# Optimization experiments

Hardware: AMD Instinct MI355X
Metric: run time of the kernel (lower is better)

Reference implementation:

```python
import jax, jax.numpy as jnp
import numpy as np

D = 2  # NUM_DIM (spatial dimension)


def _mlp(x, params, activate_final=False):
    n = len(params)
    for i, (w, b) in enumerate(params):
        x = x @ w + b
        if i < n - 1 or activate_final:
            x = jnp.tanh(x)
    return x


def _glorot(key, shape):
    fan_in, fan_out = shape[0], shape[-1]
    lim = np.sqrt(6.0 / (fan_in + fan_out)).astype(np.float32)
    return jax.random.uniform(key, shape, jnp.float32, -lim, lim)


def setup_inputs() -> dict:
    key = jax.random.key(0)
    ks = iter(jax.random.split(key, 40))
    B, N, M, K, P, C = 4, 32, 64, 16, 128, 2
    AW, TW, W = 64, 256, 128
    inp = {}
    inp['phase_coords'] = jax.random.normal(next(ks), (B, N, 2 * D), jnp.float32)
    inp['boundary_coords'] = jax.random.normal(next(ks), (B, M, 2 * D), jnp.float32)
    inp['boundary'] = jax.random.uniform(next(ks), (B, M), jnp.float32)
    inp['boundary_weights'] = jax.random.uniform(next(ks), (B, M), jnp.float32)
    inp['position_coords'] = jax.random.normal(next(ks), (B, P, D), jnp.float32)
    inp['sigma'] = jax.random.uniform(next(ks), (B, P, C), jnp.float32)
    inp['velocity_coords'] = jax.random.normal(next(ks), (B, K, D), jnp.float32)
    inp['velocity_weights'] = jax.random.uniform(next(ks), (B, K), jnp.float32)
    inp['scattering_kernel'] = jax.random.uniform(next(ks), (B, N, K), jnp.float32)
    inp['self_scattering_kernel'] = jax.random.uniform(next(ks), (B, K, K), jnp.float32)
    # attention MLP: input 2*D + 2 (coords ++ local frame) -> [64, 64, 1]
    inp['aw0'] = _glorot(next(ks), (2 * D + 2, AW)); inp['ab0'] = jnp.zeros((AW,), jnp.float32)
    inp['aw1'] = _glorot(next(ks), (AW, AW)); inp['ab1'] = jnp.zeros((AW,), jnp.float32)
    inp['aw2'] = _glorot(next(ks), (AW, 1)); inp['ab2'] = jnp.zeros((1,), jnp.float32)
    # transport MLP: input 4*D + C -> [256, 256, 128], activate_final=True
    inp['tw0'] = _glorot(next(ks), (4 * D + C, TW)); inp['tb0'] = jnp.zeros((TW,), jnp.float32)
    inp['tw1'] = _glorot(next(ks), (TW, TW)); inp['tb1'] = jnp.zeros((TW,), jnp.float32)
    inp['tw2'] = _glorot(next(ks), (TW, W)); inp['tb2'] = jnp.zeros((W,), jnp.float32)
    # scattering modules: res_block_depth=2 -> one stacked layer + one final layer
    inp['sw0'] = _glorot(next(ks), (W, W))
    inp['sb0'] = jax.random.uniform(next(ks), (W,), jnp.float32, -0.1, 0.1)
    inp['sw1'] = _glorot(next(ks), (W, W))
    inp['sb1'] = jax.random.uniform(next(ks), (W,), jnp.float32, -0.1, 0.1)
    inp['out_w'] = jax.random.uniform(next(ks), (W,), jnp.float32, -0.1, 0.1)
    return inp


def _forward(phase_coords, boundary_coords, boundary, boundary_weights,
             position_coords, sigma, velocity_coords, velocity_weights,
             scattering_kernel, self_scattering_kernel,
             aw0, ab0, aw1, ab1, aw2, ab2,
             tw0, tb0, tw1, tb1, tw2, tb2,
             sw0, sb0, sw1, sb1, out_w):
    B, N, _ = phase_coords.shape
    M = boundary_coords.shape[1]
    K = velocity_coords.shape[1]
    P = position_coords.shape[1]
    C = sigma.shape[-1]
    K1 = K + 1  # phase velocity v plus the Nv quadrature velocities

    x, v = phase_coords[..., :D], phase_coords[..., D:]          # (B,N,D)
    xp, vp = boundary_coords[..., :D], boundary_coords[..., D:]  # (B,M,D)

    # all velocities at which the transport MLP is evaluated: (B,N,K1,D)
    vall = jnp.concatenate(
        [v[:, :, None, :],
         jnp.broadcast_to(velocity_coords[:, None, :, :], (B, N, K, D))], axis=2)

    # ---- CoefficientNet (geometry-masked MLP attention over coeff positions) ----
    coords = jnp.concatenate(
        [jnp.broadcast_to(x[:, :, None, :], (B, N, K1, D)), vall], axis=-1)  # (B,N,K1,2D)
    ang_g = vall / jnp.sqrt(jnp.sum(vall ** 2, axis=-1, keepdims=True) + 1e-16)
    rel = x[:, :, None, :] - position_coords[:, None, :, :]                 # (B,N,P,D)
    rel_dist = jnp.sqrt(jnp.sum(rel ** 2, axis=-1) + 1e-16)                 # (B,N,P)
    pos_local = jnp.einsum('bnpd,bnkd->bnkp', rel, ang_g)                   # (B,N,K1,P)
    ang_local = pos_local / (rel_dist[:, :, None, :] + 1e-8)
    frames = jnp.stack([ang_local, pos_local], axis=-1)                     # (B,N,K1,P,2)
    qk = jnp.concatenate(
        [jnp.broadcast_to(coords[:, :, :, None, :], (B, N, K1, P, 2 * D)), frames], axis=-1)
    logits = _mlp(qk, [(aw0, ab0), (aw1, ab1), (aw2, ab2)])[..., 0]         # (B,N,K1,P)
    attn_w = jax.nn.softmax(jnp.where(pos_local > 0, logits, -1e30), axis=-1)
    coeff = jnp.exp(-jnp.einsum('bnkp,bpc->bnkc', attn_w, sigma))           # (B,N,K1,C)

    # ---- TransportModule: MLP + exp over (B,N,M,K1) ----
    t_in = jnp.concatenate([
        jnp.broadcast_to(x[:, :, None, None, :], (B, N, M, K1, D)),
        jnp.broadcast_to(vall[:, :, None, :, :], (B, N, M, K1, D)),
        jnp.broadcast_to(xp[:, None, :, None, :], (B, N, M, K1, D)),
        jnp.broadcast_to(vp[:, None, :, None, :], (B, N, M, K1, D)),
        jnp.broadcast_to(coeff[:, :, None, :, :], (B, N, M, K1, C)),
    ], axis=-1)
    g = jnp.exp(_mlp(t_in, [(tw0, tb0), (tw1, tb1), (tw2, tb2)], activate_final=True))
    act_v = g[:, :, :, 0, :]       # (B,N,M,W)  at the phase velocity
    act_vstar = g[:, :, :, 1:, :]  # (B,N,M,K,W) at the quadrature velocities

    rw_v = (1.0 - scattering_kernel) * velocity_weights[:, None, :]        # (B,N,K)
    rw_vs = (1.0 - self_scattering_kernel) * velocity_weights[:, None, :]  # (B,K,K)

    def scat_v(act, sw, sb):
        res = jnp.einsum('bnk,bnmkw->bnmw', rw_v, act)
        return jnp.tanh(jnp.einsum('iw,bnmw->bnmi', sw, res) + sb)

    def scat_vs(act, sw, sb):
        res = jnp.einsum('bij,bnmjw->bnmiw', rw_vs, act)
        return jnp.tanh(jnp.einsum('iw,bnmkw->bnmki', sw, res) + sb)

    # layer_stack block (res_block_depth - 1 = 1 layer, shared params within the layer)
    new_v = act_v + scat_v(act_vstar, sw0, sb0)
    act_vstar = act_vstar + scat_vs(act_vstar, sw0, sb0)
    act_v = new_v
    # final scattering module (fresh params) updating act_v with res_weights_v
    green = act_v + scat_v(act_vstar, sw1, sb1)

    gdot = jnp.einsum('bnmw,w->bnm', green, out_w)
    # quadrature over boundary points
    return jnp.einsum('bnm,bm->bn', gdot, boundary * boundary_weights)


def reference(phase_coords, boundary_coords, boundary, boundary_weights,
              position_coords, sigma, velocity_coords, velocity_weights,
              scattering_kernel, self_scattering_kernel,
              aw0, ab0, aw1, ab1, aw2, ab2,
              tw0, tb0, tw1, tb1, tw2, tb2,
              sw0, sb0, sw1, sb1, out_w):
    return _forward(phase_coords, boundary_coords, boundary, boundary_weights,
                    position_coords, sigma, velocity_coords, velocity_weights,
                    scattering_kernel, self_scattering_kernel,
                    aw0, ab0, aw1, ab1, aw2, ab2,
                    tw0, tb0, tw1, tb1, tw2, tb2,
                    sw0, sb0, sw1, sb1, out_w)
```

## Files before the change

### kernel.cpp

```cpp
#include <hip/hip_runtime.h>
#include <hip/hip_bf16.h>

#define BB 4
#define NN 32
#define MM 64
#define KK 16
#define KK1 17
#define PP 128
#define CC 2

typedef unsigned short ushort_t;
typedef unsigned int uint32;
typedef __attribute__((ext_vector_type(8))) short bhalf8;
typedef __attribute__((ext_vector_type(4))) float floatx4;

__device__ __forceinline__ float fast_tanh(float x) {
    float e = __expf(2.0f * x);
    return 1.0f - 2.0f / (e + 1.0f);
}
__device__ __forceinline__ ushort_t f2b(float f) {
    uint32 u = __float_as_uint(f);
    return (ushort_t)((u + 0x8000u) >> 16);
}
__device__ __forceinline__ float b2f(ushort_t h) {
    return __uint_as_float(((uint32)h) << 16);
}

__global__ void prep_kernel(const float* __restrict__ tw0, const float* __restrict__ tw1,
                            const float* __restrict__ tw2, const float* __restrict__ sw0,
                            const float* __restrict__ sw1, const float* __restrict__ aw0,
                            const float* __restrict__ aw1, const float* __restrict__ tb0,
                            const float* __restrict__ bcoord,
                            ushort_t* __restrict__ W1t, ushort_t* __restrict__ W2t,
                            ushort_t* __restrict__ S0t, ushort_t* __restrict__ S1t,
                            ushort_t* __restrict__ W0a, ushort_t* __restrict__ W1a,
                            ushort_t* __restrict__ w_ws) {
    int i = blockIdx.x * 256 + threadIdx.x;
    if (i < 65536) {
        int nn = i >> 8, k = i & 255;
        W1t[i] = f2b(tw1[k * 256 + nn]);
    } else if (i < 98304) {
        int j = i - 65536; int nn = j >> 8, k = j & 255;
        W2t[j] = f2b(tw2[k * 128 + nn]);
    } else if (i < 114688) {
        S0t[i - 98304] = f2b(sw0[i - 98304]);
    } else if (i < 131072) {
        S1t[i - 114688] = f2b(sw1[i - 114688]);
    } else if (i < 133120) {
        int j = i - 131072; int nn = j >> 5, k = j & 31;
        W0a[j] = (k < 6) ? f2b(aw0[k * 64 + nn]) : (ushort_t)0;
    } else if (i < 137216) {
        int j = i - 133120; int nn = j >> 6, k = j & 63;
        W1a[j] = f2b(aw1[k * 64 + nn]);
    } else if (i < 202752) {
        int j = i - 137216;
        int m = j >> 8, c = j & 255;
        float v = bcoord[m * 4 + 0] * tw0[4 * 256 + c]
                + bcoord[m * 4 + 1] * tw0[5 * 256 + c]
                + bcoord[m * 4 + 2] * tw0[6 * 256 + c]
                + bcoord[m * 4 + 3] * tw0[7 * 256 + c]
                + tb0[c];
        w_ws[j] = f2b(v);
    }
}

#define AH0S 72

__global__ __launch_bounds__(128, 4) void attn_kernel(
    const float* __restrict__ phase, const float* __restrict__ posc,
    const float* __restrict__ sigma, const float* __restrict__ velc,
    const ushort_t* __restrict__ W0a, const ushort_t* __restrict__ W1a,
    const float* __restrict__ ab0, const float* __restrict__ ab1,
    const float* __restrict__ aw2, const float* __restrict__ ab2,
    const float* __restrict__ tw0, ushort_t* __restrict__ u_ws)
{
    __shared__ __align__(16) ushort_t sAH[128 * AH0S];
    __shared__ float sPL[128];
    __shared__ float sLG[128];
    __shared__ float s_red[8];

    const int tid = threadIdx.x;
    const int wave = tid >> 6;
    const int lane = tid & 63;
    const int lrow = lane & 15;
    const int lkg  = lane >> 4;

    const int blk = blockIdx.x;
    const int b = blk / (NN * KK1);
    const int rem = blk % (NN * KK1);
    const int n = rem / KK1;
    const int k = rem % KK1;

    float x0, x1, va0, va1;
    {
        const int p = tid;
        x0 = phase[(b * NN + n) * 4 + 0];
        x1 = phase[(b * NN + n) * 4 + 1];
        if (k == 0) { va0 = phase[(b * NN + n) * 4 + 2]; va1 = phase[(b * NN + n) * 4 + 3]; }
        else { va0 = velc[(b * KK + (k - 1)) * 2 + 0]; va1 = velc[(b * KK + (k - 1)) * 2 + 1]; }
        const float inv = rsqrtf(va0 * va0 + va1 * va1 + 1e-16f);
        const float ag0 = va0 * inv, ag1 = va1 * inv;
        const float px = posc[(b * PP + p) * 2 + 0];
        const float py = posc[(b * PP + p) * 2 + 1];
        const float r0 = x0 - px, r1 = x1 - py;
        const float rd = sqrtf(r0 * r0 + r1 * r1 + 1e-16f);
        const float pl = r0 * ag0 + r1 * ag1;
        const float al = pl / (rd + 1e-8f);
        sPL[p] = pl;
        bhalf8 f0;
        f0[0] = (short)f2b(x0); f0[1] = (short)f2b(x1);
        f0[2] = (short)f2b(va0); f0[3] = (short)f2b(va1);
        f0[4] = (short)f2b(al); f0[5] = (short)f2b(pl);
        f0[6] = 0; f0[7] = 0;
        bhalf8 z = {0, 0, 0, 0, 0, 0, 0, 0};
        *(bhalf8*)&sAH[p * 32 + 0] = f0;
        *(bhalf8*)&sAH[p * 32 + 8] = z;
        *(bhalf8*)&sAH[p * 32 + 16] = z;
        *(bhalf8*)&sAH[p * 32 + 24] = z;
    }
    __syncthreads();

    {
        float b0v[4];
        #pragma unroll
        for (int j = 0; j < 4; ++j) b0v[j] = ab0[j * 16 + lrow];
        bhalf8 a[4];
        #pragma unroll
        for (int mtl = 0; mtl < 4; ++mtl)
            a[mtl] = *(const bhalf8*)&sAH[(wave * 64 + mtl * 16 + lrow) * 32 + lkg * 8];
        __syncthreads();
        #pragma unroll
        for (int j = 0; j < 4; ++j) {
            bhalf8 bf = *(const bhalf8*)(W0a + (j * 16 + lrow) * 32 + lkg * 8);
            #pragma unroll
            for (int mtl = 0; mtl < 4; ++mtl) {
                floatx4 c = {0.f, 0.f, 0.f, 0.f};
                c = __builtin_amdgcn_mfma_f32_16x16x32_bf16(a[mtl], bf, c, 0, 0, 0);
                #pragma unroll
                for (int q = 0; q < 4; ++q) {
                    int row = wave * 64 + mtl * 16 + lkg * 4 + q;
                    sAH[row * AH0S + j * 16 + lrow] = f2b(fast_tanh(c[q] + b0v[j]));
                }
            }
        }
    }
    __syncthreads();

    {
        float b1v[4], w2v[4];
        #pragma unroll
        for (int j = 0; j < 4; ++j) { b1v[j] = ab1[j * 16 + lrow]; w2v[j] = aw2[j * 16 + lrow]; }
        bhalf8 a0[4], a1[4];
        #pragma unroll
        for (int mtl = 0; mtl < 4; ++mtl) {
            int base = (wave * 64 + mtl * 16 + lrow) * AH0S;
            a0[mtl] = *(const bhalf8*)&sAH[base + lkg * 8];
            a1[mtl] = *(const bhalf8*)&sAH[base + 32 + lkg * 8];
        }
        float s[4][4];
        #pragma unroll
        for (int mtl = 0; mtl < 4; ++mtl)
            #pragma unroll
            for (int q = 0; q < 4; ++q) s[mtl][q] = 0.0f;
        #pragma unroll
        for (int j = 0; j < 4; ++j) {
            bhalf8 bf0 = *(const bhalf8*)(W1a + (j * 16 + lrow) * 64 + lkg * 8);
            bhalf8 bf1 = *(const bhalf8*)(W1a + (j * 16 + lrow) * 64 + 32 + lkg * 8);
            #pragma unroll
            for (int mtl = 0; mtl < 4; ++mtl) {
                floatx4 c = {0.f, 0.f, 0.f, 0.f};
                c = __builtin_amdgcn_mfma_f32_16x16x32_bf16(a0[mtl], bf0, c, 0, 0, 0);
                c = __builtin_amdgcn_mfma_f32_16x16x32_bf16(a1[mtl], bf1, c, 0, 0, 0);
                #pragma unroll
                for (int q = 0; q < 4; ++q)
                    s[mtl][q] += fast_tanh(c[q] + b1v[j]) * w2v[j];
            }
        }
        #pragma unroll
        for (int mask = 1; mask <= 8; mask <<= 1)
            #pragma unroll
            for (int mtl = 0; mtl < 4; ++mtl)
                #pragma unroll
                for (int q = 0; q < 4; ++q)
                    s[mtl][q] += __shfl_xor(s[mtl][q], mask, 64);
        if (lrow == 0) {
            #pragma unroll
            for (int mtl = 0; mtl < 4; ++mtl)
                #pragma unroll
                for (int q = 0; q < 4; ++q)
                    sLG[wave * 64 + mtl * 16 + lkg * 4 + q] = s[mtl][q];
        }
    }
    __syncthreads();

    {
        const int p = tid;
        const float ml = (sPL[p] > 0.0f) ? (sLG[p] + ab2[0]) : -1e30f;
        const int wid = wave;
        float mv = ml;
        for (int o = 32; o > 0; o >>= 1) mv = fmaxf(mv, __shfl_xor(mv, o, 64));
        if (lane == 0) s_red[wid] = mv;
        __syncthreads();
        mv = fmaxf(s_red[0], s_red[1]);

        const float ew = __expf(ml - mv);
        float sv = ew;
        for (int o = 32; o > 0; o >>= 1) sv += __shfl_xor(sv, o, 64);
        if (lane == 0) s_red[2 + wid] = sv;
        __syncthreads();
        sv = s_red[2] + s_red[3];
        const float attn = ew / sv;

        float s0 = attn * sigma[(b * PP + p) * 2 + 0];
        float s1 = attn * sigma[(b * PP + p) * 2 + 1];
        for (int o = 32; o > 0; o >>= 1) { s0 += __shfl_xor(s0, o, 64); s1 += __shfl_xor(s1, o, 64); }
        if (lane == 0) { s_red[4 + wid] = s0; s_red[6 + wid] = s1; }
        __syncthreads();

        const float cc0 = __expf(-(s_red[4] + s_red[5]));
        const float cc1 = __expf(-(s_red[6] + s_red[7]));
        const int ubase = ((b * NN + n) * KK1 + k) * 256;
        for (int cc = tid; cc < 256; cc += 128) {
            float uv = x0 * tw0[cc] + x1 * tw0[256 + cc]
                     + va0 * tw0[512 + cc] + va1 * tw0[768 + cc]
                     + cc0 * tw0[2048 + cc] + cc1 * tw0[2304 + cc];
            u_ws[ubase + cc] = f2b(uv);
        }
    }
}

#define H0S  136
#define H1S  264
#define GTSs 40
#define AS2S 136
#define V2S  40

#define U_H0A  0
#define U_GTS  0
#define U_GV   5128
#define U_NEWV 5384
#define U_A2S  5640
#define U_H1A  6152
#define U_AS2  6152
#define U_A3   6152
#define U_AS   15128
#define U_V2T  15128
#define F_BBW  10128
#define F_RED  10130

__global__ __launch_bounds__(256, 4) void transport_kernel(
    const float* __restrict__ boundary, const float* __restrict__ bweights,
    const float* __restrict__ vweights, const float* __restrict__ scat,
    const float* __restrict__ selfscat,
    const ushort_t* __restrict__ W1t, const ushort_t* __restrict__ W2t,
    const ushort_t* __restrict__ S0t, const ushort_t* __restrict__ S1t,
    const float* __restrict__ tb1, const float* __restrict__ tb2,
    const float* __restrict__ sb0, const float* __restrict__ sb1,
    const float* __restrict__ outw,
    const ushort_t* __restrict__ u_ws, const ushort_t* __restrict__ w_ws,
    float* __restrict__ out)
{
    __shared__ __align__(16) ushort_t smem[20268];
    float* smf = (float*)smem;

    const int tid = threadIdx.x;
    const int wave = tid >> 6;
    const int lane = tid & 63;
    const int lrow = lane & 15;
    const int lkg  = lane >> 4;

    const int blk = blockIdx.x;
    const int b  = blk >> 10;
    const int n  = (blk >> 5) & 31;
    const int mg = blk & 31;
    const int m0 = mg * 2;
    const int bn = b * NN + n;

    if (tid < 2)
        smf[F_BBW + tid] = boundary[b * MM + m0 + tid] * bweights[b * MM + m0 + tid];

    for (int idx = tid; idx < 17 * 32; idx += 256) {
        int i = idx >> 5, c = idx & 31;
        float val = 0.0f;
        if (c < 16) {
            float vw = vweights[b * KK + c];
            val = (i < 16) ? (1.0f - selfscat[(b * KK + i) * KK + c]) * vw
                           : (1.0f - scat[bn * KK + c]) * vw;
        }
        smem[U_AS + idx] = f2b(val);
    }

    floatx4 c1[4][3];
    #pragma unroll
    for (int j = 0; j < 4; ++j)
        #pragma unroll
        for (int mt = 0; mt < 3; ++mt) c1[j][mt] = (floatx4){0.f, 0.f, 0.f, 0.f};

    for (int chunk = 0; chunk < 2; ++chunk) {
        if (chunk) __syncthreads();
        for (int idx = tid; idx < 34 * 16; idx += 256) {
            int row = idx >> 4, oct = idx & 15;
            int ml = (row >= 17);
            int k = row - ml * 17;
            bhalf8 uu = *(const bhalf8*)(u_ws + (bn * KK1 + k) * 256 + chunk * 128 + oct * 8);
            bhalf8 ww = *(const bhalf8*)(w_ws + (b * MM + m0 + ml) * 256 + chunk * 128 + oct * 8);
            bhalf8 hh;
            #pragma unroll
            for (int jj = 0; jj < 8; ++jj)
                hh[jj] = (short)f2b(fast_tanh(b2f((ushort_t)uu[jj]) + b2f((ushort_t)ww[jj])));
            *(bhalf8*)&smem[U_H0A + row * H0S + oct * 8] = hh;
        }
        __syncthreads();
        #pragma unroll
        for (int ksl = 0; ksl < 4; ++ksl) {
            bhalf8 a[3];
            #pragma unroll
            for (int mt = 0; mt < 3; ++mt)
                a[mt] = *(const bhalf8*)&smem[U_H0A + (mt * 16 + lrow) * H0S + ksl * 32 + lkg * 8];
            #pragma unroll
            for (int j = 0; j < 4; ++j) {
                bhalf8 bf = *(const bhalf8*)(W1t + ((4 * wave + j) * 16 + lrow) * 256
                                             + chunk * 128 + ksl * 32 + lkg * 8);
                #pragma unroll
                for (int mt = 0; mt < 3; ++mt)
                    c1[j][mt] = __builtin_amdgcn_mfma_f32_16x16x32_bf16(a[mt], bf, c1[j][mt], 0, 0, 0);
            }
        }
    }
    {
        #pragma unroll
        for (int j = 0; j < 4; ++j) {
            float bb = tb1[(4 * wave + j) * 16 + lrow];
            #pragma unroll
            for (int mt = 0; mt < 3; ++mt)
                #pragma unroll
                for (int q = 0; q < 4; ++q) {
                    int row = mt * 16 + lkg * 4 + q;
                    if (row < 34)
                        smem[U_H1A + row * H1S + (4 * wave + j) * 16 + lrow] =
                            f2b(fast_tanh(c1[j][mt][q] + bb));
                }
        }
    }
    __syncthreads();

    for (int idx = tid; idx < 1032; idx += 256) {
        int pos = (idx < 1024) ? ((idx >> 3) * GTSs + 32 + (idx & 7)) : (5120 + idx - 1024);
        smem[U_GTS + pos] = 0;
    }
    {
        floatx4 c2[2][3];
        #pragma unroll
        for (int j = 0; j < 2; ++j)
            #pragma unroll
            for (int mt = 0; mt < 3; ++mt) c2[j][mt] = (floatx4){0.f, 0.f, 0.f, 0.f};
        #pragma unroll
        for (int ks = 0; ks < 8; ++ks) {
            bhalf8 a[3];
            #pragma unroll
            for (int mt = 0; mt < 3; ++mt)
                a[mt] = *(const bhalf8*)&smem[U_H1A + (mt * 16 + lrow) * H1S + ks * 32 + lkg * 8];
            #pragma unroll
            for (int j = 0; j < 2; ++j) {
                bhalf8 bf = *(const bhalf8*)(W2t + ((2 * wave + j) * 16 + lrow) * 256 + ks * 32 + lkg * 8);
                #pragma unroll
                for (int mt = 0; mt < 3; ++mt)
                    c2[j][mt] = __builtin_amdgcn_mfma_f32_16x16x32_bf16(a[mt], bf, c2[j][mt], 0, 0, 0);
            }
        }
        #pragma unroll
        for (int j = 0; j < 2; ++j) {
            float bb = tb2[(2 * wave + j) * 16 + lrow];
            #pragma unroll
            for (int mt = 0; mt < 3; ++mt)
                #pragma unroll
                for (int q = 0; q < 4; ++q) {
                    int row = mt * 16 + lkg * 4 + q;
                    if (row < 34) {
                        int ml = (row >= 17);
                        int k = row - ml * 17;
                        int col = (2 * wave + j) * 16 + lrow;
                        float g = __expf(fast_tanh(c2[j][mt][q] + bb));
                        if (k == 0) smem[U_GV + ml * 128 + col] = f2b(g);
                        else        smem[U_GTS + col * GTSs + ml * 16 + (k - 1)] = f2b(g);
                    }
                }
        }
    }
    __syncthreads();

    for (int idx = tid; idx < 512; idx += 256) {
        int r = idx >> 5, c = idx & 31;
        smem[U_A2S + idx] = ((c >> 4) == r) ? smem[U_AS + 16 * 32 + (c & 15)] : (ushort_t)0;
    }
    {
        bhalf8 a0 = *(const bhalf8*)&smem[U_AS + lrow * 32 + lkg * 8];
        bhalf8 a1 = *(const bhalf8*)&smem[U_AS + (16 + lrow) * 32 + lkg * 8];
        for (int m = 0; m < 2; ++m) {
            #pragma unroll
            for (int j = 0; j < 2; ++j) {
                int nt = 2 * wave + j;
                bhalf8 bf = *(const bhalf8*)&smem[U_GTS + (nt * 16 + lrow) * GTSs + m * 16 + lkg * 8];
                #pragma unroll
                for (int mt = 0; mt < 2; ++mt) {
                    floatx4 c = {0.f, 0.f, 0.f, 0.f};
                    c = __builtin_amdgcn_mfma_f32_16x16x32_bf16(mt ? a1 : a0, bf, c, 0, 0, 0);
                    #pragma unroll
                    for (int q = 0; q < 4; ++q) {
                        int ic = mt * 16 + lkg * 4 + q;
                        if (ic < 17) {
                            int r2 = (ic == 16) ? m * 17 : m * 17 + 1 + ic;
                            smem[U_AS2 + r2 * AS2S + nt * 16 + lrow] = f2b(c[q]);
                        }
                    }
                }
            }
        }
    }
    __syncthreads();

    {
        floatx4 c3[2][3];
        #pragma unroll
        for (int j = 0; j < 2; ++j)
            #pragma unroll
            for (int mt = 0; mt < 3; ++mt) c3[j][mt] = (floatx4){0.f, 0.f, 0.f, 0.f};
        #pragma unroll
        for (int ks = 0; ks < 4; ++ks) {
            bhalf8 a[3];
            #pragma unroll
            for (int mt = 0; mt < 3; ++mt)
                a[mt] = *(const bhalf8*)&smem[U_AS2 + (mt * 16 + lrow) * AS2S + ks * 32 + lkg * 8];
            #pragma unroll
            for (int j = 0; j < 2; ++j) {
                bhalf8 bf = *(const bhalf8*)(S0t + ((2 * wave + j) * 16 + lrow) * 128 + ks * 32 + lkg * 8);
                #pragma unroll
                for (int mt = 0; mt < 3; ++mt)
                    c3[j][mt] = __builtin_amdgcn_mfma_f32_16x16x32_bf16(a[mt], bf, c3[j][mt], 0, 0, 0);
            }
        }
        #pragma unroll
        for (int j = 0; j < 2; ++j) {
            float bb = sb0[(2 * wave + j) * 16 + lrow];
            #pragma unroll
            for (int mt = 0; mt < 3; ++mt)
                #pragma unroll
                for (int q = 0; q < 4; ++q) {
                    int r2 = mt * 16 + lkg * 4 + q;
                    if (r2 < 34) {
                        int m = (r2 >= 17);
                        int i2 = r2 - m * 17;
                        int col = (2 * wave + j) * 16 + lrow;
                        float val = fast_tanh(c3[j][mt][q] + bb);
                        if (i2 == 0) {
                            smem[U_NEWV + m * 128 + col] =
                                f2b(b2f(smem[U_GV + m * 128 + col]) + val);
                        } else {
                            int j2 = i2 - 1;
                            smem[U_V2T + col * V2S + m * 16 + j2] =
                                f2b(b2f(smem[U_GTS + col * GTSs + m * 16 + j2]) + val);
                        }
                    }
                }
        }
    }
    __syncthreads();

    {
        bhalf8 a = *(const bhalf8*)&smem[U_A2S + lrow * 32 + lkg * 8];
        #pragma unroll
        for (int j = 0; j < 2; ++j) {
            int nt = 2 * wave + j;
            bhalf8 bf = *(const bhalf8*)&smem[U_V2T + (nt * 16 + lrow) * V2S + lkg * 8];
            floatx4 c = {0.f, 0.f, 0.f, 0.f};
            c = __builtin_amdgcn_mfma_f32_16x16x32_bf16(a, bf, c, 0, 0, 0);
            #pragma unroll
            for (int q = 0; q < 4; ++q) {
                int r = lkg * 4 + q;
                smem[U_A3 + r * AS2S + nt * 16 + lrow] = f2b(c[q]);
            }
        }
    }
    __syncthreads();

    float acc = 0.0f;
    {
        bhalf8 a[4];
        #pragma unroll
        for (int ks = 0; ks < 4; ++ks)
            a[ks] = *(const bhalf8*)&smem[U_A3 + lrow * AS2S + ks * 32 + lkg * 8];
        #pragma unroll
        for (int j = 0; j < 2; ++j) {
            int nt = 2 * wave + j;
            float s1v = sb1[nt * 16 + lrow];
            float owv = outw[nt * 16 + lrow];
            floatx4 c = {0.f, 0.f, 0.f, 0.f};
            #pragma unroll
            for (int ks = 0; ks < 4; ++ks) {
                bhalf8 bf = *(const bhalf8*)(S1t + (nt * 16 + lrow) * 128 + ks * 32 + lkg * 8);
                c = __builtin_amdgcn_mfma_f32_16x16x32_bf16(a[ks], bf, c, 0, 0, 0);
            }
            #pragma unroll
            for (int q = 0; q < 4; ++q) {
                int r = lkg * 4 + q;
                if (r < 2) {
                    int col = nt * 16 + lrow;
                    float green = b2f(smem[U_NEWV + r * 128 + col]) + fast_tanh(c[q] + s1v);
                    acc += green * owv * smf[F_BBW + r];
                }
            }
        }
    }
    for (int o = 32; o > 0; o >>= 1) acc += __shfl_xor(acc, o, 64);
    if (lane == 0) smf[F_RED + wave] = acc;
    __syncthreads();
    if (tid == 0) {
        float tot = smf[F_RED + 0] + smf[F_RED + 1] + smf[F_RED + 2] + smf[F_RED + 3];
        atomicAdd(&out[bn], tot);
    }
}

extern "C" void kernel_launch(void* const* d_in, const int* in_sizes, int n_in,
                              void* d_out, int out_size, void* d_ws, size_t ws_size,
                              hipStream_t stream) {
    const float* phase    = (const float*)d_in[0];
    const float* bcoord   = (const float*)d_in[1];
    const float* boundary = (const float*)d_in[2];
    const float* bweights = (const float*)d_in[3];
    const float* posc     = (const float*)d_in[4];
    const float* sigma    = (const float*)d_in[5];
    const float* velc     = (const float*)d_in[6];
    const float* vweights = (const float*)d_in[7];
    const float* scat     = (const float*)d_in[8];
    const float* selfscat = (const float*)d_in[9];
    const float* aw0 = (const float*)d_in[10];
    const float* ab0 = (const float*)d_in[11];
    const float* aw1 = (const float*)d_in[12];
    const float* ab1 = (const float*)d_in[13];
    const float* aw2 = (const float*)d_in[14];
    const float* ab2 = (const float*)d_in[15];
    const float* tw0 = (const float*)d_in[16];
    const float* tb0 = (const float*)d_in[17];
    const float* tw1 = (const float*)d_in[18];
    const float* tb1 = (const float*)d_in[19];
    const float* tw2 = (const float*)d_in[20];
    const float* tb2 = (const float*)d_in[21];
    const float* sw0 = (const float*)d_in[22];
    const float* sb0 = (const float*)d_in[23];
    const float* sw1 = (const float*)d_in[24];
    const float* sb1 = (const float*)d_in[25];
    const float* outw = (const float*)d_in[26];

    float* out = (float*)d_out;
    char* ws = (char*)d_ws;
    ushort_t* W1t  = (ushort_t*)(ws + 0);
    ushort_t* W2t  = (ushort_t*)(ws + 131072);
    ushort_t* S0t  = (ushort_t*)(ws + 196608);
    ushort_t* S1t  = (ushort_t*)(ws + 229376);
    ushort_t* W0a  = (ushort_t*)(ws + 262144);
    ushort_t* W1a  = (ushort_t*)(ws + 266240);
    ushort_t* u_ws = (ushort_t*)(ws + 274432);
    ushort_t* w_ws = (ushort_t*)(ws + 1388544);

    hipMemsetAsync(d_out, 0, (size_t)out_size * sizeof(float), stream);

    prep_kernel<<<792, 256, 0, stream>>>(tw0, tw1, tw2, sw0, sw1, aw0, aw1, tb0, bcoord,
                                         W1t, W2t, S0t, S1t, W0a, W1a, w_ws);

    attn_kernel<<<BB * NN * KK1, 128, 0, stream>>>(
        phase, posc, sigma, velc, W0a, W1a, ab0, ab1, aw2, ab2, tw0, u_ws);

    transport_kernel<<<BB * NN * 32, 256, 0, stream>>>(
        boundary, bweights, vweights, scat, selfscat,
        W1t, W2t, S0t, S1t, tb1, tb2, sb0, sb1, outw, u_ws, w_ws, out);
}
```

Before: 283.8 us.

## Shrink shared memory to allow five blocks per CU and restructure tanh staging

Reorganizes the LDS layout so the kernel needs less shared memory (U_V2T and the float scratch slots move), and raises the launch bound from 4 to 5 blocks per CU to increase occupancy. The first-layer tanh staging loop becomes a fixed per-thread assignment of rows with all loads issued up front, and the zero-fill uses vector stores. A-operand reads for rows beyond 34 are clamped to row 32 so they never touch the shrunken, now-overlapping region. The changes risk register pressure from the tighter launch bound and rely on the new overlapping LDS regions having non-conflicting lifetimes.

```diff
diff --git a/kernel.cpp b/kernel.cpp
--- a/kernel.cpp
+++ b/kernel.cpp
@@ -24,6 +24,14 @@
 }
 __device__ __forceinline__ float b2f(ushort_t h) {
     return __uint_as_float(((uint32)h) << 16);
+}
+
+__device__ __forceinline__ bhalf8 tanh_uw(bhalf8 u, bhalf8 w) {
+    bhalf8 h;
+    #pragma unroll
+    for (int j = 0; j < 8; ++j)
+        h[j] = (short)f2b(fast_tanh(b2f((ushort_t)u[j]) + b2f((ushort_t)w[j])));
+    return h;
 }
 
 __global__ void prep_kernel(const float* __restrict__ tw0, const float* __restrict__ tw1,
@@ -243,12 +251,12 @@
 #define U_H1A  6152
 #define U_AS2  6152
 #define U_A3   6152
+#define U_V2T  10776
 #define U_AS   15128
-#define U_V2T  15128
-#define F_BBW  10128
-#define F_RED  10130
-
-__global__ __launch_bounds__(256, 4) void transport_kernel(
+#define F_BBW  7960
+#define F_RED  7962
+
+__global__ __launch_bounds__(256, 5) void transport_kernel(
     const float* __restrict__ boundary, const float* __restrict__ bweights,
     const float* __restrict__ vweights, const float* __restrict__ scat,
     const float* __restrict__ selfscat,
@@ -260,7 +268,7 @@
     const ushort_t* __restrict__ u_ws, const ushort_t* __restrict__ w_ws,
     float* __restrict__ out)
 {
-    __shared__ __align__(16) ushort_t smem[20268];
+    __shared__ __align__(16) ushort_t smem[16160];
     float* smf = (float*)smem;
 
     const int tid = threadIdx.x;
@@ -298,17 +306,25 @@
 
     for (int chunk = 0; chunk < 2; ++chunk) {
         if (chunk) __syncthreads();
-        for (int idx = tid; idx < 34 * 16; idx += 256) {
-            int row = idx >> 4, oct = idx & 15;
-            int ml = (row >= 17);
-            int k = row - ml * 17;
-            bhalf8 uu = *(const bhalf8*)(u_ws + (bn * KK1 + k) * 256 + chunk * 128 + oct * 8);
-            bhalf8 ww = *(const bhalf8*)(w_ws + (b * MM + m0 + ml) * 256 + chunk * 128 + oct * 8);
-            bhalf8 hh;
-            #pragma unroll
-            for (int jj = 0; jj < 8; ++jj)
-                hh[jj] = (short)f2b(fast_tanh(b2f((ushort_t)uu[jj]) + b2f((ushort_t)ww[jj])));
-            *(bhalf8*)&smem[U_H0A + row * H0S + oct * 8] = hh;
+        {
+            const int r0  = tid >> 4;
+            const int oct = tid & 15;
+            const int co  = chunk * 128 + oct * 8;
+            const bhalf8 u0 = *(const bhalf8*)(u_ws + (bn * KK1 + r0) * 256 + co);
+            const bhalf8 w0 = *(const bhalf8*)(w_ws + (b * MM + m0) * 256 + co);
+            const int ml1 = (r0 >= 1) ? 1 : 0;
+            const int k1  = r0 + 16 - 17 * ml1;
+            const bhalf8 u1 = *(const bhalf8*)(u_ws + (bn * KK1 + k1) * 256 + co);
+            const bhalf8 w1 = *(const bhalf8*)(w_ws + (b * MM + m0 + ml1) * 256 + co);
+            bhalf8 u2, w2;
+            if (r0 < 2) {
+                u2 = *(const bhalf8*)(u_ws + (bn * KK1 + 15 + r0) * 256 + co);
+                w2 = *(const bhalf8*)(w_ws + (b * MM + m0 + 1) * 256 + co);
+            }
+            *(bhalf8*)&smem[U_H0A + r0 * H0S + oct * 8]        = tanh_uw(u0, w0);
+            *(bhalf8*)&smem[U_H0A + (16 + r0) * H0S + oct * 8] = tanh_uw(u1, w1);
+            if (r0 < 2)
+                *(bhalf8*)&smem[U_H0A + (32 + r0) * H0S + oct * 8] = tanh_uw(u2, w2);
         }
         __syncthreads();
         #pragma unroll
@@ -344,9 +360,10 @@
     }
     __syncthreads();
 
-    for (int idx = tid; idx < 1032; idx += 256) {
-        int pos = (idx < 1024) ? ((idx >> 3) * GTSs + 32 + (idx & 7)) : (5120 + idx - 1024);
-        smem[U_GTS + pos] = 0;
+    {
+        bhalf8 z = {0, 0, 0, 0, 0, 0, 0, 0};
+        if (tid < 128)       *(bhalf8*)&smem[U_GTS + tid * GTSs + 32] = z;
+        else if (tid == 128) *(bhalf8*)&smem[U_GTS + 5120] = z;
     }
     {
         floatx4 c2[2][3];
@@ -358,8 +375,11 @@
         for (int ks = 0; ks < 8; ++ks) {
             bhalf8 a[3];
             #pragma unroll
-            for (int mt = 0; mt < 3; ++mt)
-                a[mt] = *(const bhalf8*)&smem[U_H1A + (mt * 16 + lrow) * H1S + ks * 32 + lkg * 8];
+            for (int mt = 0; mt < 3; ++mt) {
+                int rr = mt * 16 + lrow;
+                if (rr >= 34) rr = 32;
+                a[mt] = *(const bhalf8*)&smem[U_H1A + rr * H1S + ks * 32 + lkg * 8];
+            }
             #pragma unroll
             for (int j = 0; j < 2; ++j) {
                 bhalf8 bf = *(const bhalf8*)(W2t + ((2 * wave + j) * 16 + lrow) * 256 + ks * 32 + lkg * 8);
```

New measurement: 300.3 us. 5.8% more time.
